# Kernel optimization log

Measured on AMD Instinct MI355X. Metric: run time of the kernel, lower is better.

## Reference

```python
import jax, jax.numpy as jnp
import numpy as np

# Blur config (matches init_kwargs)
BLUR_K = [1, 3, 3, 1]
PAD = (2, 1)
UPSAMPLE_FACTOR = 2
UP = 1    # Blur.call uses upfirdn2d defaults: up=1, down=1
DOWN = 1


def make_kernel(k):
    k = np.array(k, dtype=np.float32)
    if k.ndim == 1:
        k = k[:, None] * k[None, :]
    k /= np.sum(k)
    return k


def setup_inputs() -> dict:
    key = jax.random.key(0)
    x = jax.random.normal(key, (8, 128, 256, 256), dtype=jnp.float32)
    k = make_kernel(BLUR_K) * (UPSAMPLE_FACTOR ** 2)  # [4,4] FIR kernel
    kernel = jnp.asarray(k, dtype=jnp.float32)
    return {"x": x, "kernel": kernel}


def reference(x, kernel):
    # upfirdn2d(x, kernel, up=1, down=1, pad=(2,1)) on NCHW input.
    # The TF code flips the kernel then runs tf.nn.conv2d (correlation),
    # i.e. true convolution with the FIR kernel. lax conv is correlation,
    # so we pass the flipped kernel to match exactly.
    B, C, H, W = x.shape
    kh, kw = kernel.shape
    kflip = kernel[::-1, ::-1].reshape(1, 1, kh, kw)  # OIHW, single channel
    # Fold channels into batch: each channel filtered independently.
    y = jax.lax.conv_general_dilated(
        x.reshape(B * C, 1, H, W),
        kflip,
        window_strides=(DOWN, DOWN),
        padding=((PAD[0], PAD[1]), (PAD[0], PAD[1])),
        lhs_dilation=(UP, UP),  # zero-insert upsampling (no-op for UP=1)
        dimension_numbers=("NCHW", "OIHW", "NCHW"),
    )
    _, _, Ho, Wo = y.shape  # (H*UP + pad0 + pad1 - kh)//DOWN + 1 = 256
    return y.reshape(B, C, Ho, Wo)
```

## Files before the change

### kernel.cpp

```cpp
#include <hip/hip_runtime.h>


#define HH 256
#define WW 256

__global__ __launch_bounds__(256) void blur_kernel(
    const float* __restrict__ x, const float* __restrict__ k4,
    float* __restrict__ out)
{
    const int tid   = threadIdx.x;
    const int cx    = tid & 63;
    const int ry    = tid >> 6;
    const int j     = cx << 2;
    const int chunk = blockIdx.x;
    const int plane = blockIdx.y;
    const int i0    = chunk * 32 + ry * 8;

    float Kr[4][4];
#pragma unroll
    for (int u = 0; u < 4; ++u)
#pragma unroll
        for (int t = 0; t < 4; ++t)
            Kr[u][t] = k4[u * 4 + (3 - t)];

    const float* xp = x + (size_t)plane * (HH * WW);

    float acc[8][4];
#pragma unroll
    for (int r = 0; r < 8; ++r)
#pragma unroll
        for (int c = 0; c < 4; ++c) acc[r][c] = 0.f;

#pragma unroll
    for (int rr = 0; rr < 11; ++rr) {
        const int r = i0 - 2 + rr;
        float w0, w1, w2, w3, w4, w5, w6;
        if ((unsigned)r < (unsigned)HH) {
            const float* row = xp + r * WW + j;
            if (j >= 2) {
                float2 l = *(const float2*)(row - 2);
                w0 = l.x; w1 = l.y;
            } else { w0 = 0.f; w1 = 0.f; }
            float4 m = *(const float4*)(row);
            w2 = m.x; w3 = m.y; w4 = m.z; w5 = m.w;
            w6 = (j + 4 < WW) ? row[4] : 0.f;
        } else {
            w0 = w1 = w2 = w3 = w4 = w5 = w6 = 0.f;
        }
        const float wv[7] = {w0, w1, w2, w3, w4, w5, w6};
#pragma unroll
        for (int u = 0; u < 4; ++u) {
            const int lo = rr + u - 3;
            if (lo >= 0 && lo < 8) {
#pragma unroll
                for (int c = 0; c < 4; ++c)
#pragma unroll
                    for (int t = 0; t < 4; ++t)
                        acc[lo][c] += Kr[u][t] * wv[c + t];
            }
        }
    }

    float* op = out + (size_t)plane * (HH * WW) + (size_t)i0 * WW + j;
#pragma unroll
    for (int r = 0; r < 8; ++r) {
        *(float4*)(op + (size_t)r * WW) =
            make_float4(acc[r][0], acc[r][1], acc[r][2], acc[r][3]);
    }
}

extern "C" void kernel_launch(void* const* d_in, const int* in_sizes, int n_in,
                              void* d_out, int out_size, void* d_ws, size_t ws_size,
                              hipStream_t stream) {
    const float* x = (const float*)d_in[0];
    const float* k = (const float*)d_in[1];
    float* out = (float*)d_out;

    dim3 grid(8, 1024);
    blur_kernel<<<grid, 256, 0, stream>>>(x, k, out);
}
```

Baseline: 440.3 us.

## Stage input row tile with halo in shared memory before blur compute

Each block now loads its 35-row input slab, including halo rows and zero-padded columns, into LDS using coalesced float4 loads with clamped, masked boundaries. Warps then read their seven-wide windows from shared memory instead of issuing overlapping unaligned global loads per row. This removes redundant global traffic from halo rows shared between warps and from the misaligned edge loads. In exchange it adds about 37 KB of LDS per block and a barrier, which may limit occupancy, and LDS reads at 4-float lane strides may cause bank conflicts.

Measured after the change: 432.1 us. Within noise of the previous version (-1.9%).

```diff
diff --git a/kernel.cpp b/kernel.cpp
--- a/kernel.cpp
+++ b/kernel.cpp
@@ -3,18 +3,24 @@
 
 #define HH 256
 #define WW 256
+#define TR 32
+#define LR (TR + 3)
+#define LSTR 264
 
 __global__ __launch_bounds__(256) void blur_kernel(
     const float* __restrict__ x, const float* __restrict__ k4,
     float* __restrict__ out)
 {
+    __shared__ float tile[LR * LSTR];
+
     const int tid   = threadIdx.x;
-    const int cx    = tid & 63;
-    const int ry    = tid >> 6;
-    const int j     = cx << 2;
+    const int lane  = tid & 63;
+    const int warp  = tid >> 6;
     const int chunk = blockIdx.x;
     const int plane = blockIdx.y;
-    const int i0    = chunk * 32 + ry * 8;
+    const int i0    = chunk * TR;
+
+    const float* xp = x + (size_t)plane * (HH * WW);
 
     float Kr[4][4];
 #pragma unroll
@@ -23,7 +29,29 @@
         for (int t = 0; t < 4; ++t)
             Kr[u][t] = k4[u * 4 + (3 - t)];
 
-    const float* xp = x + (size_t)plane * (HH * WW);
+    for (int idx = tid; idx < LR * 8; idx += 256) {
+        const int row = idx >> 3, c8 = idx & 7;
+        const int col = (c8 < 4) ? c8 : (260 + (c8 - 4));
+        tile[row * LSTR + col] = 0.f;
+    }
+
+    float4 v[9];
+#pragma unroll
+    for (int k = 0; k < 9; ++k) {
+        const int l  = warp + 4 * k;
+        const int g  = i0 - 2 + l;
+        const int gc = min(max(g, 0), HH - 1);
+        v[k] = *(const float4*)(xp + (size_t)gc * WW + 4 * lane);
+        if (g != gc) v[k] = make_float4(0.f, 0.f, 0.f, 0.f);
+    }
+#pragma unroll
+    for (int k = 0; k < 9; ++k) {
+        const int l = warp + 4 * k;
+        if (l < LR)
+            *(float4*)(&tile[l * LSTR + 4 + 4 * lane]) = v[k];
+    }
+
+    __syncthreads();
 
     float acc[8][4];
 #pragma unroll
@@ -31,23 +59,11 @@
 #pragma unroll
         for (int c = 0; c < 4; ++c) acc[r][c] = 0.f;
 
+    const int obase = warp * 8;
 #pragma unroll
     for (int rr = 0; rr < 11; ++rr) {
-        const int r = i0 - 2 + rr;
-        float w0, w1, w2, w3, w4, w5, w6;
-        if ((unsigned)r < (unsigned)HH) {
-            const float* row = xp + r * WW + j;
-            if (j >= 2) {
-                float2 l = *(const float2*)(row - 2);
-                w0 = l.x; w1 = l.y;
-            } else { w0 = 0.f; w1 = 0.f; }
-            float4 m = *(const float4*)(row);
-            w2 = m.x; w3 = m.y; w4 = m.z; w5 = m.w;
-            w6 = (j + 4 < WW) ? row[4] : 0.f;
-        } else {
-            w0 = w1 = w2 = w3 = w4 = w5 = w6 = 0.f;
-        }
-        const float wv[7] = {w0, w1, w2, w3, w4, w5, w6};
+        const float* p = &tile[(obase + rr) * LSTR + 4 * lane + 2];
+        const float wv[7] = {p[0], p[1], p[2], p[3], p[4], p[5], p[6]};
 #pragma unroll
         for (int u = 0; u < 4; ++u) {
             const int lo = rr + u - 3;
@@ -61,12 +77,12 @@
         }
     }
 
-    float* op = out + (size_t)plane * (HH * WW) + (size_t)i0 * WW + j;
+    float* op = out + (size_t)plane * (HH * WW)
+                    + (size_t)(i0 + obase) * WW + 4 * lane;
 #pragma unroll
-    for (int r = 0; r < 8; ++r) {
+    for (int r = 0; r < 8; ++r)
         *(float4*)(op + (size_t)r * WW) =
             make_float4(acc[r][0], acc[r][1], acc[r][2], acc[r][3]);
-    }
 }
 
 extern "C" void kernel_launch(void* const* d_in, const int* in_sizes, int n_in,
```
